# Performance work log

Hardware: AMD Instinct MI355X
Metric: run time of the kernel (lower is better)

Reference implementation:

```python
import jax, jax.numpy as jnp
import numpy as np

DIM = 256
NUM_HEADS = 8
HEAD_DIM = DIM // NUM_HEADS          # 32
KEY_DIM = int(HEAD_DIM * 0.5)        # 16
SCALE = KEY_DIM ** (-0.5)
QKV_OUT = DIM + 2 * KEY_DIM * NUM_HEADS  # 512
BN_EPS = 1e-3


def _bn(x, gamma, beta, mean, var):
    # inference-mode BatchNorm2d over channel axis 1 of NCHW
    inv = gamma / jnp.sqrt(var + BN_EPS)
    return x * inv[None, :, None, None] + (beta - mean * inv)[None, :, None, None]


def _conv1x1(x, w):
    # w: (O, C, 1, 1)
    return jnp.einsum('bchw,oc->bohw', x, w[:, :, 0, 0])


def _dwconv3x3(x, w):
    # depthwise 3x3, SAME padding; w: (C, 1, 3, 3)
    return jax.lax.conv_general_dilated(
        x, w, window_strides=(1, 1), padding='SAME',
        feature_group_count=x.shape[1],
        dimension_numbers=('NCHW', 'OIHW', 'NCHW'))


def setup_inputs() -> dict:
    key = jax.random.key(0)
    ks = jax.random.split(key, 16)
    B, C, H, W = 16, DIM, 32, 32
    inp = {
        'x': jax.random.normal(ks[0], (B, C, H, W), jnp.float32),
        'qkv_w': jax.random.normal(ks[1], (QKV_OUT, DIM, 1, 1), jnp.float32) * (1.0 / np.sqrt(DIM)),
        'qkv_gamma': jnp.ones((QKV_OUT,), jnp.float32),
        'qkv_beta': jnp.zeros((QKV_OUT,), jnp.float32),
        'qkv_mean': jax.random.normal(ks[2], (QKV_OUT,), jnp.float32) * 0.1,
        'qkv_var': jax.random.uniform(ks[3], (QKV_OUT,), jnp.float32, 0.5, 1.5),
        'pe_w': jax.random.normal(ks[4], (DIM, 1, 3, 3), jnp.float32) * (1.0 / 3.0),
        'pe_gamma': jnp.ones((DIM,), jnp.float32),
        'pe_beta': jnp.zeros((DIM,), jnp.float32),
        'pe_mean': jax.random.normal(ks[5], (DIM,), jnp.float32) * 0.1,
        'pe_var': jax.random.uniform(ks[6], (DIM,), jnp.float32, 0.5, 1.5),
        'proj_w': jax.random.normal(ks[7], (DIM, DIM, 1, 1), jnp.float32) * (1.0 / np.sqrt(DIM)),
        'proj_gamma': jnp.ones((DIM,), jnp.float32),
        'proj_beta': jnp.zeros((DIM,), jnp.float32),
        'proj_mean': jax.random.normal(ks[8], (DIM,), jnp.float32) * 0.1,
        'proj_var': jax.random.uniform(ks[9], (DIM,), jnp.float32, 0.5, 1.5),
    }
    return inp


def reference(x, qkv_w, qkv_gamma, qkv_beta, qkv_mean, qkv_var,
              pe_w, pe_gamma, pe_beta, pe_mean, pe_var,
              proj_w, proj_gamma, proj_beta, proj_mean, proj_var):
    B, C, H, W = x.shape
    N = H * W
    # qkv: 1x1 conv + BN (act=False)
    qkv = _bn(_conv1x1(x, qkv_w), qkv_gamma, qkv_beta, qkv_mean, qkv_var)
    qkv = qkv.reshape(B, NUM_HEADS, 2 * KEY_DIM + HEAD_DIM, N)
    q = qkv[:, :, :KEY_DIM]                          # (B, h, kd, N)
    k = qkv[:, :, KEY_DIM:2 * KEY_DIM]               # (B, h, kd, N)
    v = qkv[:, :, 2 * KEY_DIM:]                      # (B, h, hd, N)
    # attn = (q^T @ k) * scale, softmax over last dim
    attn = jnp.einsum('bhdn,bhdm->bhnm', q, k) * SCALE   # (B, h, N, N)
    attn = jax.nn.softmax(attn, axis=-1)
    # v @ attn^T
    v_attn = jnp.einsum('bhdn,bhmn->bhdm', v, attn)      # (B, h, hd, N)
    v_attn = v_attn.reshape(B, C, H, W)
    v_reshaped = v.reshape(B, C, H, W)
    pos_enc = _bn(_dwconv3x3(v_reshaped, pe_w), pe_gamma, pe_beta, pe_mean, pe_var)
    out = v_attn + pos_enc
    out = _bn(_conv1x1(out, proj_w), proj_gamma, proj_beta, proj_mean, proj_var)
    return out
```

## Files before the change

### kernel.cpp

```cpp
#include <hip/hip_runtime.h>

#define B_ 16
#define C_ 256
#define N_ 1024
#define NH 8
#define HD 32
#define KD 16
#define QKV_OUT_ 512
#define BN_EPS 1e-3f
#define SCALE2_ (0.25f * 1.44269504088896f)

typedef __attribute__((ext_vector_type(8))) short short8;
typedef __attribute__((ext_vector_type(16))) float float16;

__device__ inline unsigned short f2bf(float f) {
  unsigned int u = __float_as_uint(f);
  return (unsigned short)((u + 0x7FFF + ((u >> 16) & 1)) >> 16);
}
__device__ inline float bf2f(unsigned short s) {
  return __uint_as_float(((unsigned int)s) << 16);
}
__device__ inline float16 zero16() {
  float16 z;
  #pragma unroll
  for (int i = 0; i < 16; ++i) z[i] = 0.f;
  return z;
}
__device__ inline unsigned int pack_bf16_trunc(float a, float b) {
  return __builtin_amdgcn_perm(__float_as_uint(b), __float_as_uint(a), 0x07060302u);
}
__device__ inline unsigned int pack_bf16_rne(float a, float b) {
  return (unsigned int)f2bf(a) | ((unsigned int)f2bf(b) << 16);
}
__device__ inline float fast_exp2(float x) {
#if __has_builtin(__builtin_amdgcn_exp2f)
  return __builtin_amdgcn_exp2f(x);
#else
  return exp2f(x);
#endif
}
__device__ inline void pl32(unsigned int& a, unsigned int& b) {
#if __has_builtin(__builtin_amdgcn_permlane32_swap)
  typedef __attribute__((ext_vector_type(2))) int int2v;
  int2v r = __builtin_amdgcn_permlane32_swap((int)a, (int)b, false, false);
  a = (unsigned int)r[0];
  b = (unsigned int)r[1];
#else
  unsigned int ea = (unsigned int)__shfl_xor((int)a, 32, 64);
  unsigned int eb = (unsigned int)__shfl_xor((int)b, 32, 64);
  bool hi = (threadIdx.x & 32) != 0;
  unsigned int an = hi ? eb : a;
  unsigned int bn = hi ? b : ea;
  a = an; b = bn;
#endif
}
__device__ inline short8 lds_frag(const unsigned short* p) {
  union { uint2 u[2]; short8 s; } r;
  r.u[0] = *(const uint2*)p;
  r.u[1] = *(const uint2*)(p + 4);
  return r.s;
}
__device__ inline void lds_store16(unsigned short* p, uint4 v) {
  *(uint2*)p = make_uint2(v.x, v.y);
  *(uint2*)(p + 4) = make_uint2(v.z, v.w);
}

__global__ __launch_bounds__(256) void fold_weights(
    const float* __restrict__ qkv_w, const float* __restrict__ qg,
    const float* __restrict__ qb, const float* __restrict__ qm,
    const float* __restrict__ qv,
    const float* __restrict__ proj_w, const float* __restrict__ pg,
    const float* __restrict__ pb, const float* __restrict__ pm,
    const float* __restrict__ pv,
    unsigned short* __restrict__ wq, float* __restrict__ biasq,
    unsigned short* __restrict__ wp, float* __restrict__ biasp)
{
  const int o = blockIdx.x, c = threadIdx.x;
  if (o < QKV_OUT_) {
    float s = ((o & 63) < 16) ? SCALE2_ : 1.f;
    float inv = qg[o] * rsqrtf(qv[o] + BN_EPS) * s;
    wq[o * C_ + c] = f2bf(qkv_w[o * C_ + c] * inv);
    if (c == 0) biasq[o] = qb[o] * s - qm[o] * inv;
  } else {
    int oo = o - QKV_OUT_;
    float inv = pg[oo] * rsqrtf(pv[oo] + BN_EPS);
    wp[oo * C_ + c] = f2bf(proj_w[oo * C_ + c] * inv);
    if (c == 0) biasp[oo] = pb[oo] - pm[oo] * inv;
  }
}

__global__ __launch_bounds__(256) void gemm_qkv(
    const float* __restrict__ x, const unsigned short* __restrict__ wq,
    const float* __restrict__ bias,
    unsigned short* __restrict__ qkT, unsigned short* __restrict__ vbuf)
{
  constexpr int STR = 44;
  __shared__ __align__(8) unsigned short wa[2][128 * STR];
  __shared__ __align__(8) unsigned short xb[2][128 * STR];
  const int tid = threadIdx.x;
  const int wave = tid >> 6, lane = tid & 63, l31 = lane & 31, lh = lane >> 5;
  const int wm = wave & 1, wn = wave >> 1;
  const int b = blockIdx.x >> 3, nloc = (blockIdx.x & 7) * 128;
  const int o0 = blockIdx.y * 128;

  const int r0 = tid >> 2, oc0 = (tid & 3) * 8;
  const int r1 = r0 + 64;
  const int tok = tid & 127, chalf = (tid >> 7) * 16;
  const float* xbase = x + (size_t)b * C_ * N_ + nloc + tok;

  uint4 ga0, ga1;
  float nb[16];

  auto loadk = [&](int kc) {
    ga0 = *(const uint4*)(wq + (size_t)(o0 + r0) * C_ + kc * 32 + oc0);
    ga1 = *(const uint4*)(wq + (size_t)(o0 + r1) * C_ + kc * 32 + oc0);
    #pragma unroll
    for (int j = 0; j < 16; ++j)
      nb[j] = xbase[(size_t)(kc * 32 + chalf + j) * N_];
  };
  auto storek = [&](int bufi) {
    lds_store16(&wa[bufi][r0 * STR + oc0], ga0);
    lds_store16(&wa[bufi][r1 * STR + oc0], ga1);
    unsigned int pk[8];
    #pragma unroll
    for (int q = 0; q < 8; ++q) pk[q] = pack_bf16_rne(nb[2 * q], nb[2 * q + 1]);
    lds_store16(&xb[bufi][tok * STR + chalf], make_uint4(pk[0], pk[1], pk[2], pk[3]));
    lds_store16(&xb[bufi][tok * STR + chalf + 8], make_uint4(pk[4], pk[5], pk[6], pk[7]));
  };

  float16 acc[2][2];
  #pragma unroll
  for (int i = 0; i < 2; ++i)
    #pragma unroll
    for (int j = 0; j < 2; ++j) acc[i][j] = zero16();

  loadk(0);
  storek(0);
  __syncthreads();

  for (int kc = 0; kc < 8; ++kc) {
    const int buf = kc & 1;
    if (kc < 7) loadk(kc + 1);

    #pragma unroll
    for (int ks = 0; ks < 2; ++ks) {
      const int ko = ks * 16 + lh * 8;
      short8 a0 = lds_frag(&wa[buf][(wm * 64 + l31) * STR + ko]);
      short8 a1 = lds_frag(&wa[buf][(wm * 64 + 32 + l31) * STR + ko]);
      short8 b0 = lds_frag(&xb[buf][(wn * 64 + l31) * STR + ko]);
      short8 b1 = lds_frag(&xb[buf][(wn * 64 + 32 + l31) * STR + ko]);
      acc[0][0] = __builtin_amdgcn_mfma_f32_32x32x16_bf16(a0, b0, acc[0][0], 0, 0, 0);
      acc[0][1] = __builtin_amdgcn_mfma_f32_32x32x16_bf16(a0, b1, acc[0][1], 0, 0, 0);
      acc[1][0] = __builtin_amdgcn_mfma_f32_32x32x16_bf16(a1, b0, acc[1][0], 0, 0, 0);
      acc[1][1] = __builtin_amdgcn_mfma_f32_32x32x16_bf16(a1, b1, acc[1][1], 0, 0, 0);
    }

    if (kc < 7) storek(buf ^ 1);
    __syncthreads();
  }

  const int hh = (o0 >> 6) + wm;
  #pragma unroll
  for (int bn = 0; bn < 2; ++bn) {
    int n = nloc + wn * 64 + bn * 32 + l31;
    unsigned short* row = qkT + (((size_t)b * NH + hh) * N_ + n) * 32;
    #pragma unroll
    for (int qd = 0; qd < 4; ++qd) {
      int cc0 = 8 * qd + 4 * lh;
      ushort4 rv;
      rv.x = f2bf(acc[0][bn][4 * qd + 0] + bias[hh * 64 + cc0 + 0]);
      rv.y = f2bf(acc[0][bn][4 * qd + 1] + bias[hh * 64 + cc0 + 1]);
      rv.z = f2bf(acc[0][bn][4 * qd + 2] + bias[hh * 64 + cc0 + 2]);
      rv.w = f2bf(acc[0][bn][4 * qd + 3] + bias[hh * 64 + cc0 + 3]);
      *(ushort4*)(row + cc0) = rv;
    }
  }
  #pragma unroll
  for (int r = 0; r < 16; ++r) {
    int d = (r & 3) + 8 * (r >> 2) + 4 * lh;
    float bo = bias[hh * 64 + 32 + d];
    unsigned short* vrow =
        vbuf + ((size_t)b * C_ + hh * 32 + d) * N_ + nloc + wn * 64 + l31;
    #pragma unroll
    for (int bn = 0; bn < 2; ++bn)
      vrow[bn * 32] = f2bf(acc[1][bn][r] + bo);
  }
}

__global__ __launch_bounds__(256) void gemm_proj(
    const unsigned short* __restrict__ inT, const unsigned short* __restrict__ wfold,
    const float* __restrict__ bias, float* __restrict__ outf)
{
  constexpr int STR = 44;
  __shared__ __align__(8) unsigned short wa[2][128 * STR];
  __shared__ __align__(8) unsigned short xb[2][128 * STR];
  const int tid = threadIdx.x;
  const int wave = tid >> 6, lane = tid & 63, l31 = lane & 31, lh = lane >> 5;
  const int wm = wave & 1, wn = wave >> 1;
  const int n0g = blockIdx.x * 128;
  const int o0 = blockIdx.y * 128;
  const int b = n0g >> 10, nloc = n0g & 1023;

  const int r0 = tid >> 2, oc0 = (tid & 3) * 8;
  const int r1 = r0 + 64;

  float16 acc[2][2];
  #pragma unroll
  for (int i = 0; i < 2; ++i)
    #pragma unroll
    for (int j = 0; j < 2; ++j) acc[i][j] = zero16();

  uint4 ga0, ga1, gb0, gb1;
  auto loadk = [&](int kc) {
    ga0 = *(const uint4*)(wfold + (size_t)(o0 + r0) * C_ + kc * 32 + oc0);
    ga1 = *(const uint4*)(wfold + (size_t)(o0 + r1) * C_ + kc * 32 + oc0);
    gb0 = *(const uint4*)(inT + (size_t)(n0g + r0) * C_ + kc * 32 + oc0);
    gb1 = *(const uint4*)(inT + (size_t)(n0g + r1) * C_ + kc * 32 + oc0);
  };
  auto storek = [&](int bufi) {
    lds_store16(&wa[bufi][r0 * STR + oc0], ga0);
    lds_store16(&wa[bufi][r1 * STR + oc0], ga1);
    lds_store16(&xb[bufi][r0 * STR + oc0], gb0);
    lds_store16(&xb[bufi][r1 * STR + oc0], gb1);
  };

  loadk(0);
  storek(0);
  __syncthreads();

  for (int kc = 0; kc < 8; ++kc) {
    const int buf = kc & 1;
    if (kc < 7) loadk(kc + 1);

    #pragma unroll
    for (int ks = 0; ks < 2; ++ks) {
      const int ko = ks * 16 + lh * 8;
      short8 a0 = lds_frag(&wa[buf][(wm * 64 + l31) * STR + ko]);
      short8 a1 = lds_frag(&wa[buf][(wm * 64 + 32 + l31) * STR + ko]);
      short8 b0 = lds_frag(&xb[buf][(wn * 64 + l31) * STR + ko]);
      short8 b1 = lds_frag(&xb[buf][(wn * 64 + 32 + l31) * STR + ko]);
      acc[0][0] = __builtin_amdgcn_mfma_f32_32x32x16_bf16(a0, b0, acc[0][0], 0, 0, 0);
      acc[0][1] = __builtin_amdgcn_mfma_f32_32x32x16_bf16(a0, b1, acc[0][1], 0, 0, 0);
      acc[1][0] = __builtin_amdgcn_mfma_f32_32x32x16_bf16(a1, b0, acc[1][0], 0, 0, 0);
      acc[1][1] = __builtin_amdgcn_mfma_f32_32x32x16_bf16(a1, b1, acc[1][1], 0, 0, 0);
    }

    if (kc < 7) storek(buf ^ 1);
    __syncthreads();
  }

  #pragma unroll
  for (int am = 0; am < 2; ++am) {
    #pragma unroll
    for (int r = 0; r < 16; ++r) {
      int o = o0 + wm * 64 + am * 32 + (r & 3) + 8 * (r >> 2) + 4 * lh;
      float bo = bias[o];
      float* orow = outf + ((size_t)b * C_ + o) * N_ + nloc + wn * 64 + l31;
      #pragma unroll
      for (int bn = 0; bn < 2; ++bn)
        orow[bn * 32] = acc[am][bn][r] + bo;
    }
  }
}

__global__ __launch_bounds__(256) void dwconv_bn(
    const unsigned short* __restrict__ vbuf, const float* __restrict__ pw,
    const float* __restrict__ gamma, const float* __restrict__ beta,
    const float* __restrict__ mean, const float* __restrict__ var,
    unsigned short* __restrict__ posb)
{
  __shared__ float t[34][34];
  const int c = blockIdx.x, b = blockIdx.y;
  const int tid = threadIdx.x;
  const unsigned short* vp = vbuf + ((size_t)b * C_ + c) * N_;

  #pragma unroll
  for (int r = 0; r < 4; ++r) {
    int idx = r * 256 + tid;
    t[(idx >> 5) + 1][(idx & 31) + 1] = bf2f(vp[idx]);
  }
  if (tid < 34) {
    t[0][tid] = 0.f; t[33][tid] = 0.f;
    t[tid][0] = 0.f; t[tid][33] = 0.f;
  }
  __syncthreads();

  float w9[9];
  #pragma unroll
  for (int i = 0; i < 9; ++i) w9[i] = pw[c * 9 + i];
  float inv = gamma[c] * rsqrtf(var[c] + BN_EPS);
  float add = beta[c] - mean[c] * inv;

  unsigned short* op = posb + ((size_t)b * C_ + c) * N_;
  #pragma unroll
  for (int r = 0; r < 4; ++r) {
    int idx = r * 256 + tid;
    int y = idx >> 5, x = idx & 31;
    float s = 0.f;
    #pragma unroll
    for (int dy = 0; dy < 3; ++dy)
      #pragma unroll
      for (int dx = 0; dx < 3; ++dx)
        s += t[y + dy][x + dx] * w9[dy * 3 + dx];
    op[idx] = f2bf(s * inv + add);
  }
}

__global__ __launch_bounds__(256) void attn_mfma(
    const unsigned short* __restrict__ qkT, const unsigned short* __restrict__ vbuf,
    const unsigned short* __restrict__ posb, unsigned short* __restrict__ vattnT)
{
  __shared__ __align__(8) unsigned short k_lds[2][128 * 28];
  __shared__ __align__(8) unsigned short v_lds[2][32 * 140];

  const int tid = threadIdx.x;
  const int wave = tid >> 6, lane = tid & 63;
  const int l31 = lane & 31, lh = lane >> 5;
  const int b = blockIdx.x >> 3, h = blockIdx.x & 7;
  const int qbase = blockIdx.y * 128 + wave * 32;

  const unsigned short* qkb = qkT + ((size_t)b * NH + h) * N_ * 32;
  const unsigned short* vhead = vbuf + ((size_t)b * C_ + h * HD) * N_;

  const int skey = tid >> 1, shalf = tid & 1;
  const int svd = tid >> 3, svseg = tid & 7;

  short8 qf = lds_frag(qkb + (size_t)(qbase + l31) * 32 + lh * 8);

  uint4 gk, gv0, gv1;
  auto loadc = [&](int kc) {
    gk  = *(const uint4*)(qkb + (size_t)(kc + skey) * 32 + 16 + shalf * 8);
    gv0 = *(const uint4*)(vhead + (size_t)svd * N_ + kc + svseg * 16);
    gv1 = *(const uint4*)(vhead + (size_t)svd * N_ + kc + svseg * 16 + 8);
  };
  auto storec = [&](int bufi) {
    lds_store16(&k_lds[bufi][skey * 28 + shalf * 8], gk);
    lds_store16(&v_lds[bufi][svd * 140 + svseg * 16], gv0);
    lds_store16(&v_lds[bufi][svd * 140 + svseg * 16 + 8], gv1);
  };

  loadc(0);
  storec(0);
  __syncthreads();

  float16 oacc = zero16();
  float ls[4] = {0.f, 0.f, 0.f, 0.f};

  for (int c = 0; c < 8; ++c) {
    const int buf = c & 1;
    if (c < 7) loadc((c + 1) * 128);

    #pragma unroll
    for (int t = 0; t < 4; ++t) {
      const int key0 = t * 32;
      short8 kf = lds_frag(&k_lds[buf][(key0 + l31) * 28 + lh * 8]);
      float16 st = __builtin_amdgcn_mfma_f32_32x32x16_bf16(kf, qf, zero16(), 0, 0, 0);

      unsigned int u[8];
      #pragma unroll
      for (int q = 0; q < 8; ++q) {
        float pe = fast_exp2(st[2 * q]);
        float po = fast_exp2(st[2 * q + 1]);
        ls[q & 3] += pe + po;
        u[q] = pack_bf16_trunc(pe, po);
      }

      #pragma unroll
      for (int f = 0; f < 2; ++f) {
        short8 vf = lds_frag(&v_lds[buf][l31 * 140 + key0 + f * 16 + lh * 8]);
        const int q0 = f * 4;
        unsigned int a0 = u[q0], a2 = u[q0 + 2]; pl32(a0, a2);
        unsigned int a1 = u[q0 + 1], a3 = u[q0 + 3]; pl32(a1, a3);
        union { unsigned int w[4]; short8 s; } bf;
        bf.w[0] = a0; bf.w[1] = a1; bf.w[2] = a2; bf.w[3] = a3;
        oacc = __builtin_amdgcn_mfma_f32_32x32x16_bf16(vf, bf.s, oacc, 0, 0, 0);
      }
    }

    if (c < 7) storec(buf ^ 1);
    __syncthreads();
  }

  float lsum = (ls[0] + ls[1]) + (ls[2] + ls[3]);
  lsum += __shfl_xor(lsum, 32, 64);
  const float linv = 1.f / lsum;

  const int token = qbase + l31;
  float val[16];
  #pragma unroll
  for (int r = 0; r < 16; ++r) {
    int d = (r & 3) + 8 * (r >> 2) + 4 * lh;
    val[r] = oacc[r] * linv +
             bf2f(posb[((size_t)b * C_ + h * HD + d) * N_ + token]);
  }
  unsigned int u[8];
  #pragma unroll
  for (int m = 0; m < 8; ++m) u[m] = pack_bf16_rne(val[2 * m], val[2 * m + 1]);
  pl32(u[0], u[4]); pl32(u[1], u[5]); pl32(u[2], u[6]); pl32(u[3], u[7]);
  unsigned short* row = vattnT + ((size_t)b * N_ + token) * C_ + h * HD + lh * 16;
  *(uint4*)(row)     = make_uint4(u[0], u[1], u[4], u[5]);
  *(uint4*)(row + 8) = make_uint4(u[2], u[3], u[6], u[7]);
}

extern "C" void kernel_launch(void* const* d_in, const int* in_sizes, int n_in,
                              void* d_out, int out_size, void* d_ws, size_t ws_size,
                              hipStream_t stream) {
  const float* x          = (const float*)d_in[0];
  const float* qkv_w      = (const float*)d_in[1];
  const float* qkv_gamma  = (const float*)d_in[2];
  const float* qkv_beta   = (const float*)d_in[3];
  const float* qkv_mean   = (const float*)d_in[4];
  const float* qkv_var    = (const float*)d_in[5];
  const float* pe_w       = (const float*)d_in[6];
  const float* pe_gamma   = (const float*)d_in[7];
  const float* pe_beta    = (const float*)d_in[8];
  const float* pe_mean    = (const float*)d_in[9];
  const float* pe_var     = (const float*)d_in[10];
  const float* proj_w     = (const float*)d_in[11];
  const float* proj_gamma = (const float*)d_in[12];
  const float* proj_beta  = (const float*)d_in[13];
  const float* proj_mean  = (const float*)d_in[14];
  const float* proj_var   = (const float*)d_in[15];
  float* out = (float*)d_out;

  char* ws = (char*)d_ws;
  unsigned short* qkT = (unsigned short*)ws;
  ws += (size_t)B_ * NH * N_ * 32 * sizeof(unsigned short);
  unsigned short* vbuf = (unsigned short*)ws;
  ws += (size_t)B_ * C_ * N_ * sizeof(unsigned short);
  unsigned short* vattnT = (unsigned short*)ws;
  ws += (size_t)B_ * N_ * C_ * sizeof(unsigned short);
  unsigned short* posb = (unsigned short*)ws;
  ws += (size_t)B_ * C_ * N_ * sizeof(unsigned short);
  unsigned short* wq = (unsigned short*)ws;
  ws += (size_t)QKV_OUT_ * C_ * sizeof(unsigned short);
  unsigned short* wp = (unsigned short*)ws;
  ws += (size_t)C_ * C_ * sizeof(unsigned short);
  float* biasq = (float*)ws; ws += QKV_OUT_ * sizeof(float);
  float* biasp = (float*)ws;

  fold_weights<<<dim3(QKV_OUT_ + C_), 256, 0, stream>>>(
      qkv_w, qkv_gamma, qkv_beta, qkv_mean, qkv_var,
      proj_w, proj_gamma, proj_beta, proj_mean, proj_var,
      wq, biasq, wp, biasp);

  gemm_qkv<<<dim3(128, 4), 256, 0, stream>>>(x, wq, biasq, qkT, vbuf);

  dwconv_bn<<<dim3(C_, B_), 256, 0, stream>>>(
      vbuf, pe_w, pe_gamma, pe_beta, pe_mean, pe_var, posb);

  attn_mfma<<<dim3(128, 8), 256, 0, stream>>>(qkT, vbuf, posb, vattnT);

  gemm_proj<<<dim3(128, 2), 256, 0, stream>>>(vattnT, wp, biasp, out);
}
```

Before: 156.5 us.

## Pre-transpose x to bf16 and load GEMM tiles directly global-to-LDS

Adds a separate transpose kernel that converts x to a token-major bf16 layout. Both 1x1-conv GEMMs are merged into one templated kernel that fills shared memory with direct global-to-LDS loads, using a K-chunk of 64 and a single unpadded buffer instead of register-staged double buffering. The aim is to remove the strided per-token fp32 reads in the QKV GEMM and to cut register and VALU staging work. The cost is an extra kernel launch and a round trip of x through memory, loss of load/compute overlap, and possible LDS bank conflicts now that the row padding is gone.

```diff
diff --git a/kernel.cpp b/kernel.cpp
--- a/kernel.cpp
+++ b/kernel.cpp
@@ -63,6 +63,16 @@
 __device__ inline void lds_store16(unsigned short* p, uint4 v) {
   *(uint2*)p = make_uint2(v.x, v.y);
   *(uint2*)(p + 4) = make_uint2(v.z, v.w);
+}
+__device__ inline void gl2lds16(const unsigned short* g, unsigned short* l) {
+#if __has_builtin(__builtin_amdgcn_global_load_lds)
+  __builtin_amdgcn_global_load_lds(
+      (const __attribute__((address_space(1))) unsigned int*)g,
+      (__attribute__((address_space(3))) unsigned int*)l, 16, 0, 0);
+#else
+  const int lane = threadIdx.x & 63;
+  *(uint4*)((char*)l + lane * 16) = *(const uint4*)g;
+#endif
 }
 
 __global__ __launch_bounds__(256) void fold_weights(
@@ -89,111 +99,43 @@
   }
 }
 
-__global__ __launch_bounds__(256) void gemm_qkv(
-    const float* __restrict__ x, const unsigned short* __restrict__ wq,
+__global__ __launch_bounds__(256) void transpose_x(
+    const float* __restrict__ x, unsigned short* __restrict__ xT)
+{
+  __shared__ float t[64][69];
+  const int tid = threadIdx.x;
+  const int nt = blockIdx.x, ct = blockIdx.y, b = blockIdx.z;
+  const int n0 = nt * 64, c0 = ct * 64;
+
+  #pragma unroll
+  for (int it = 0; it < 4; ++it) {
+    int cl = it * 16 + (tid >> 4);
+    int nl = (tid & 15) * 4;
+    float4 v = *(const float4*)(x + ((size_t)b * C_ + c0 + cl) * N_ + n0 + nl);
+    t[cl][nl + 0] = v.x; t[cl][nl + 1] = v.y;
+    t[cl][nl + 2] = v.z; t[cl][nl + 3] = v.w;
+  }
+  __syncthreads();
+
+  const int nr = tid >> 2, cseg = (tid & 3) * 16;
+  unsigned int pk[8];
+  #pragma unroll
+  for (int q = 0; q < 8; ++q)
+    pk[q] = pack_bf16_rne(t[cseg + 2 * q][nr], t[cseg + 2 * q + 1][nr]);
+  unsigned short* row = xT + ((size_t)b * N_ + n0 + nr) * C_ + c0 + cseg;
+  *(uint4*)(row)     = make_uint4(pk[0], pk[1], pk[2], pk[3]);
+  *(uint4*)(row + 8) = make_uint4(pk[4], pk[5], pk[6], pk[7]);
+}
+
+template <int MODE>
+__global__ __launch_bounds__(256) void gemm_gl(
+    const unsigned short* __restrict__ inT, const unsigned short* __restrict__ wfold,
     const float* __restrict__ bias,
-    unsigned short* __restrict__ qkT, unsigned short* __restrict__ vbuf)
+    unsigned short* __restrict__ qkT, unsigned short* __restrict__ vbuf,
+    float* __restrict__ outf)
 {
-  constexpr int STR = 44;
-  __shared__ __align__(8) unsigned short wa[2][128 * STR];
-  __shared__ __align__(8) unsigned short xb[2][128 * STR];
-  const int tid = threadIdx.x;
-  const int wave = tid >> 6, lane = tid & 63, l31 = lane & 31, lh = lane >> 5;
-  const int wm = wave & 1, wn = wave >> 1;
-  const int b = blockIdx.x >> 3, nloc = (blockIdx.x & 7) * 128;
-  const int o0 = blockIdx.y * 128;
-
-  const int r0 = tid >> 2, oc0 = (tid & 3) * 8;
-  const int r1 = r0 + 64;
-  const int tok = tid & 127, chalf = (tid >> 7) * 16;
-  const float* xbase = x + (size_t)b * C_ * N_ + nloc + tok;
-
-  uint4 ga0, ga1;
-  float nb[16];
-
-  auto loadk = [&](int kc) {
-    ga0 = *(const uint4*)(wq + (size_t)(o0 + r0) * C_ + kc * 32 + oc0);
-    ga1 = *(const uint4*)(wq + (size_t)(o0 + r1) * C_ + kc * 32 + oc0);
-    #pragma unroll
-    for (int j = 0; j < 16; ++j)
-      nb[j] = xbase[(size_t)(kc * 32 + chalf + j) * N_];
-  };
-  auto storek = [&](int bufi) {
-    lds_store16(&wa[bufi][r0 * STR + oc0], ga0);
-    lds_store16(&wa[bufi][r1 * STR + oc0], ga1);
-    unsigned int pk[8];
-    #pragma unroll
-    for (int q = 0; q < 8; ++q) pk[q] = pack_bf16_rne(nb[2 * q], nb[2 * q + 1]);
-    lds_store16(&xb[bufi][tok * STR + chalf], make_uint4(pk[0], pk[1], pk[2], pk[3]));
-    lds_store16(&xb[bufi][tok * STR + chalf + 8], make_uint4(pk[4], pk[5], pk[6], pk[7]));
-  };
-
-  float16 acc[2][2];
-  #pragma unroll
-  for (int i = 0; i < 2; ++i)
-    #pragma unroll
-    for (int j = 0; j < 2; ++j) acc[i][j] = zero16();
-
-  loadk(0);
-  storek(0);
-  __syncthreads();
-
-  for (int kc = 0; kc < 8; ++kc) {
-    const int buf = kc & 1;
-    if (kc < 7) loadk(kc + 1);
-
-    #pragma unroll
-    for (int ks = 0; ks < 2; ++ks) {
-      const int ko = ks * 16 + lh * 8;
-      short8 a0 = lds_frag(&wa[buf][(wm * 64 + l31) * STR + ko]);
-      short8 a1 = lds_frag(&wa[buf][(wm * 64 + 32 + l31) * STR + ko]);
-      short8 b0 = lds_frag(&xb[buf][(wn * 64 + l31) * STR + ko]);
-      short8 b1 = lds_frag(&xb[buf][(wn * 64 + 32 + l31) * STR + ko]);
-      acc[0][0] = __builtin_amdgcn_mfma_f32_32x32x16_bf16(a0, b0, acc[0][0], 0, 0, 0);
-      acc[0][1] = __builtin_amdgcn_mfma_f32_32x32x16_bf16(a0, b1, acc[0][1], 0, 0, 0);
-      acc[1][0] = __builtin_amdgcn_mfma_f32_32x32x16_bf16(a1, b0, acc[1][0], 0, 0, 0);
-      acc[1][1] = __builtin_amdgcn_mfma_f32_32x32x16_bf16(a1, b1, acc[1][1], 0, 0, 0);
-    }
-
-    if (kc < 7) storek(buf ^ 1);
-    __syncthreads();
-  }
-
-  const int hh = (o0 >> 6) + wm;
-  #pragma unroll
-  for (int bn = 0; bn < 2; ++bn) {
-    int n = nloc + wn * 64 + bn * 32 + l31;
-    unsigned short* row = qkT + (((size_t)b * NH + hh) * N_ + n) * 32;
-    #pragma unroll
-    for (int qd = 0; qd < 4; ++qd) {
-      int cc0 = 8 * qd + 4 * lh;
-      ushort4 rv;
-      rv.x = f2bf(acc[0][bn][4 * qd + 0] + bias[hh * 64 + cc0 + 0]);
-      rv.y = f2bf(acc[0][bn][4 * qd + 1] + bias[hh * 64 + cc0 + 1]);
-      rv.z = f2bf(acc[0][bn][4 * qd + 2] + bias[hh * 64 + cc0 + 2]);
-      rv.w = f2bf(acc[0][bn][4 * qd + 3] + bias[hh * 64 + cc0 + 3]);
-      *(ushort4*)(row + cc0) = rv;
-    }
-  }
-  #pragma unroll
-  for (int r = 0; r < 16; ++r) {
-    int d = (r & 3) + 8 * (r >> 2) + 4 * lh;
-    float bo = bias[hh * 64 + 32 + d];
-    unsigned short* vrow =
-        vbuf + ((size_t)b * C_ + hh * 32 + d) * N_ + nloc + wn * 64 + l31;
-    #pragma unroll
-    for (int bn = 0; bn < 2; ++bn)
-      vrow[bn * 32] = f2bf(acc[1][bn][r] + bo);
-  }
-}
-
-__global__ __launch_bounds__(256) void gemm_proj(
-    const unsigned short* __restrict__ inT, const unsigned short* __restrict__ wfold,
-    const float* __restrict__ bias, float* __restrict__ outf)
-{
-  constexpr int STR = 44;
-  __shared__ __align__(8) unsigned short wa[2][128 * STR];
-  __shared__ __align__(8) unsigned short xb[2][128 * STR];
+  __shared__ __align__(16) unsigned short wa[128 * 64];
+  __shared__ __align__(16) unsigned short xb[128 * 64];
   const int tid = threadIdx.x;
   const int wave = tid >> 6, lane = tid & 63, l31 = lane & 31, lh = lane >> 5;
   const int wm = wave & 1, wn = wave >> 1;
@@ -201,8 +143,8 @@
   const int o0 = blockIdx.y * 128;
   const int b = n0g >> 10, nloc = n0g & 1023;
 
-  const int r0 = tid >> 2, oc0 = (tid & 3) * 8;
-  const int r1 = r0 + 64;
+  const int crow = lane >> 3;
+  const int cseg = (lane & 7) * 8;
 
   float16 acc[2][2];
   #pragma unroll
@@ -210,55 +152,70 @@
     #pragma unroll
     for (int j = 0; j < 2; ++j) acc[i][j] = zero16();
 
-  uint4 ga0, ga1, gb0, gb1;
-  auto loadk = [&](int kc) {
-    ga0 = *(const uint4*)(wfold + (size_t)(o0 + r0) * C_ + kc * 32 + oc0);
-    ga1 = *(const uint4*)(wfold + (size_t)(o0 + r1) * C_ + kc * 32 + oc0);
-    gb0 = *(const uint4*)(inT + (size_t)(n0g + r0) * C_ + kc * 32 + oc0);
-    gb1 = *(const uint4*)(inT + (size_t)(n0g + r1) * C_ + kc * 32 + oc0);
-  };
-  auto storek = [&](int bufi) {
-    lds_store16(&wa[bufi][r0 * STR + oc0], ga0);
-    lds_store16(&wa[bufi][r1 * STR + oc0], ga1);
-    lds_store16(&xb[bufi][r0 * STR + oc0], gb0);
-    lds_store16(&xb[bufi][r1 * STR + oc0], gb1);
-  };
-
-  loadk(0);
-  storek(0);
-  __syncthreads();
-
-  for (int kc = 0; kc < 8; ++kc) {
-    const int buf = kc & 1;
-    if (kc < 7) loadk(kc + 1);
-
-    #pragma unroll
-    for (int ks = 0; ks < 2; ++ks) {
+  for (int kc = 0; kc < 4; ++kc) {
+    __syncthreads();
+    #pragma unroll
+    for (int j = 0; j < 4; ++j) {
+      const int rbase = wave * 32 + j * 8;
+      const int row = rbase + crow;
+      gl2lds16(wfold + (size_t)(o0 + row) * C_ + kc * 64 + cseg, &wa[rbase * 64]);
+      gl2lds16(inT + (size_t)(n0g + row) * C_ + kc * 64 + cseg, &xb[rbase * 64]);
+    }
+    __syncthreads();
+
+    #pragma unroll
+    for (int ks = 0; ks < 4; ++ks) {
       const int ko = ks * 16 + lh * 8;
-      short8 a0 = lds_frag(&wa[buf][(wm * 64 + l31) * STR + ko]);
-      short8 a1 = lds_frag(&wa[buf][(wm * 64 + 32 + l31) * STR + ko]);
-      short8 b0 = lds_frag(&xb[buf][(wn * 64 + l31) * STR + ko]);
-      short8 b1 = lds_frag(&xb[buf][(wn * 64 + 32 + l31) * STR + ko]);
+      short8 a0 = *(const short8*)&wa[(wm * 64 + l31) * 64 + ko];
+      short8 a1 = *(const short8*)&wa[(wm * 64 + 32 + l31) * 64 + ko];
+      short8 b0 = *(const short8*)&xb[(wn * 64 + l31) * 64 + ko];
+      short8 b1 = *(const short8*)&xb[(wn * 64 + 32 + l31) * 64 + ko];
       acc[0][0] = __builtin_amdgcn_mfma_f32_32x32x16_bf16(a0, b0, acc[0][0], 0, 0, 0);
       acc[0][1] = __builtin_amdgcn_mfma_f32_32x32x16_bf16(a0, b1, acc[0][1], 0, 0, 0);
       acc[1][0] = __builtin_amdgcn_mfma_f32_32x32x16_bf16(a1, b0, acc[1][0], 0, 0, 0);
       acc[1][1] = __builtin_amdgcn_mfma_f32_32x32x16_bf16(a1, b1, acc[1][1], 0, 0, 0);
     }
-
-    if (kc < 7) storek(buf ^ 1);
-    __syncthreads();
-  }
-
-  #pragma unroll
-  for (int am = 0; am < 2; ++am) {
+  }
+
+  if constexpr (MODE == 0) {
+    const int hh = (o0 >> 6) + wm;
+    #pragma unroll
+    for (int bn = 0; bn < 2; ++bn) {
+      int n = nloc + wn * 64 + bn * 32 + l31;
+      unsigned short* row = qkT + (((size_t)b * NH + hh) * N_ + n) * 32;
+      #pragma unroll
+      for (int qd = 0; qd < 4; ++qd) {
+        int cc0 = 8 * qd + 4 * lh;
+        ushort4 rv;
+        rv.x = f2bf(acc[0][bn][4 * qd + 0] + bias[hh * 64 + cc0 + 0]);
+        rv.y = f2bf(acc[0][bn][4 * qd + 1] + bias[hh * 64 + cc0 + 1]);
+        rv.z = f2bf(acc[0][bn][4 * qd + 2] + bias[hh * 64 + cc0 + 2]);
+        rv.w = f2bf(acc[0][bn][4 * qd + 3] + bias[hh * 64 + cc0 + 3]);
+        *(ushort4*)(row + cc0) = rv;
+      }
+    }
     #pragma unroll
     for (int r = 0; r < 16; ++r) {
-      int o = o0 + wm * 64 + am * 32 + (r & 3) + 8 * (r >> 2) + 4 * lh;
-      float bo = bias[o];
-      float* orow = outf + ((size_t)b * C_ + o) * N_ + nloc + wn * 64 + l31;
+      int d = (r & 3) + 8 * (r >> 2) + 4 * lh;
+      float bo = bias[hh * 64 + 32 + d];
+      unsigned short* vrow =
+          vbuf + ((size_t)b * C_ + hh * 32 + d) * N_ + nloc + wn * 64 + l31;
       #pragma unroll
       for (int bn = 0; bn < 2; ++bn)
-        orow[bn * 32] = acc[am][bn][r] + bo;
+        vrow[bn * 32] = f2bf(acc[1][bn][r] + bo);
+    }
+  } else {
+    #pragma unroll
+    for (int am = 0; am < 2; ++am) {
+      #pragma unroll
+      for (int r = 0; r < 16; ++r) {
+        int o = o0 + wm * 64 + am * 32 + (r & 3) + 8 * (r >> 2) + 4 * lh;
+        float bo = bias[o];
+        float* orow = outf + ((size_t)b * C_ + o) * N_ + nloc + wn * 64 + l31;
+        #pragma unroll
+        for (int bn = 0; bn < 2; ++bn)
+          orow[bn * 32] = acc[am][bn][r] + bo;
+      }
     }
   }
 }
@@ -428,6 +385,8 @@
   ws += (size_t)B_ * NH * N_ * 32 * sizeof(unsigned short);
   unsigned short* vbuf = (unsigned short*)ws;
   ws += (size_t)B_ * C_ * N_ * sizeof(unsigned short);
+  unsigned short* xT = (unsigned short*)ws;
+  ws += (size_t)B_ * N_ * C_ * sizeof(unsigned short);
   unsigned short* vattnT = (unsigned short*)ws;
   ws += (size_t)B_ * N_ * C_ * sizeof(unsigned short);
   unsigned short* posb = (unsigned short*)ws;
@@ -444,12 +403,16 @@
       proj_w, proj_gamma, proj_beta, proj_mean, proj_var,
       wq, biasq, wp, biasp);
 
-  gemm_qkv<<<dim3(128, 4), 256, 0, stream>>>(x, wq, biasq, qkT, vbuf);
+  transpose_x<<<dim3(16, 4, 16), 256, 0, stream>>>(x, xT);
+
+  gemm_gl<0><<<dim3(128, 4), 256, 0, stream>>>(
+      xT, wq, biasq, qkT, vbuf, nullptr);
 
   dwconv_bn<<<dim3(C_, B_), 256, 0, stream>>>(
       vbuf, pe_w, pe_gamma, pe_beta, pe_mean, pe_var, posb);
 
   attn_mfma<<<dim3(128, 8), 256, 0, stream>>>(qkT, vbuf, posb, vattnT);
 
-  gemm_proj<<<dim3(128, 2), 256, 0, stream>>>(vattnT, wp, biasp, out);
-}
+  gemm_gl<1><<<dim3(128, 2), 256, 0, stream>>>(
+      vattnT, wp, biasp, nullptr, nullptr, out);
+}
```

New measurement: 161.1 us. 2.9% more time.
